# Performance work log

Hardware: AMD Instinct MI355X
Metric: run time of the kernel (lower is better)

The kernel has to match this reference:

```python
import jax, jax.numpy as jnp
import numpy as np

N, C_IN, C_OUT, T, V = 64, 64, 64, 300, 25
INTER_C = C_OUT // 4
NUM_SUBSET = 3
BN_EPS = 1e-5


def setup_inputs() -> dict:
    key = jax.random.key(0)
    ks = jax.random.split(key, 12)
    w_scale = 0.05  # keep attention logits in a sane range
    return {
        "x": jax.random.normal(ks[0], (N, C_IN, T, V), jnp.float32),
        "A": jax.random.uniform(ks[1], (NUM_SUBSET, V, V), jnp.float32),
        "graph_attn": jnp.ones((NUM_SUBSET, V, V), jnp.float32),
        "g_w": jax.random.normal(ks[2], (NUM_SUBSET, C_OUT, C_IN), jnp.float32) * w_scale,
        "g_b": jax.random.normal(ks[3], (NUM_SUBSET, C_OUT), jnp.float32) * w_scale,
        "a_w": jax.random.normal(ks[4], (NUM_SUBSET, INTER_C, C_IN), jnp.float32) * w_scale,
        "a_b": jax.random.normal(ks[5], (NUM_SUBSET, INTER_C), jnp.float32) * w_scale,
        "b_w": jax.random.normal(ks[6], (NUM_SUBSET, INTER_C, C_IN), jnp.float32) * w_scale,
        "b_b": jax.random.normal(ks[7], (NUM_SUBSET, INTER_C), jnp.float32) * w_scale,
        "bn_gamma": jax.random.uniform(ks[8], (C_OUT,), jnp.float32, 0.5, 1.5),
        "bn_beta": jax.random.normal(ks[9], (C_OUT,), jnp.float32) * 0.1,
        "bn_mean": jax.random.normal(ks[10], (C_OUT,), jnp.float32) * 0.1,
        "bn_var": jax.random.uniform(ks[11], (C_OUT,), jnp.float32, 0.5, 1.5),
    }


def _conv1x1(x, w, b):
    # 1x1 Conv2d over channel dim of [N, C, T, V]
    return jnp.einsum('nctv,oc->notv', x, w) + b[None, :, None, None]


def reference(x, A, graph_attn, g_w, g_b, a_w, a_b, b_w, b_b,
              bn_gamma, bn_beta, bn_mean, bn_var):
    A_full = A + graph_attn  # [3, V, V]
    hidden = None
    for i in range(NUM_SUBSET):
        A1 = _conv1x1(x, a_w[i], a_b[i]).transpose(0, 3, 1, 2)  # [N, V, inter_c, T]
        A2 = _conv1x1(x, b_w[i], b_b[i])                        # [N, inter_c, T, V]
        # [N, V, W, T] attention logits, softmax over axis -2 (W)
        S = jnp.einsum('nvct,nctw->nvwt', A1, A2) / INTER_C
        S = jax.nn.softmax(S, axis=-2)
        S = S + A_full[i][None, :, :, None]
        # faithful to torch: sum S over its first spatial axis, elementwise on x
        z = _conv1x1(jnp.einsum('nctv,nwvt->nctv', x, S), g_w[i], g_b[i])
        hidden = z if hidden is None else hidden + z
    # inference-mode BatchNorm2d
    inv = jax.lax.rsqrt(bn_var + BN_EPS)
    h = (hidden - bn_mean[None, :, None, None]) * (bn_gamma * inv)[None, :, None, None] \
        + bn_beta[None, :, None, None]
    # in_channels == out_channels -> identity residual
    h = h + x
    return jax.nn.relu(h)
```

## Files before the change

kernel.cpp:

```cpp
#include <hip/hip_runtime.h>
#include <hip/hip_bf16.h>
#include <math.h>


typedef __attribute__((ext_vector_type(8)))  short bf8;
typedef __attribute__((ext_vector_type(4)))  short bf4;
typedef __attribute__((ext_vector_type(4)))  float f4;
typedef __attribute__((ext_vector_type(16))) float f16v;

#define TT    5
#define COLS  125
#define COLSP 128
#define XROW  72
#define PQROW 40

#define WS_AW    0
#define WS_BW    6144
#define WS_GW    12288
#define WS_COLA  36864
#define WS_SCL   37376
#define WS_SHF   37632
#define WS_END   37888

__device__ __forceinline__ short f2bf(float f) {
  __hip_bfloat16 h = __float2bfloat16(f);
  return __builtin_bit_cast(short, h);
}
__device__ __forceinline__ float bf2f(short s) {
  union { unsigned u; float f; } v;
  v.u = ((unsigned)(unsigned short)s) << 16;
  return v.f;
}
__device__ __forceinline__ float rsum16(float v) {
  v += __shfl_xor(v, 1);
  v += __shfl_xor(v, 2);
  v += __shfl_xor(v, 4);
  v += __shfl_xor(v, 8);
  return v;
}

__global__ void tagc_prep(
    const float* __restrict__ A,    const float* __restrict__ G,
    const float* __restrict__ g_w,  const float* __restrict__ g_b,
    const float* __restrict__ a_w,  const float* __restrict__ b_w,
    const float* __restrict__ bn_g, const float* __restrict__ bn_b,
    const float* __restrict__ bn_m, const float* __restrict__ bn_v,
    short* __restrict__ aw_bf, short* __restrict__ bw_bf,
    short* __restrict__ gw_bf, float* __restrict__ colA3,
    float* __restrict__ scl,   float* __restrict__ shf2)
{
  const int b = blockIdx.x, tid = threadIdx.x;
  if (b < 12) {
    int base = b * 1024 + tid * 4;
    f4 v = *(const f4*)(g_w + base);
    bf4 o;
    #pragma unroll
    for (int r = 0; r < 4; ++r) o[r] = f2bf(v[r]);
    *(bf4*)(gw_bf + base) = o;
  } else if (b == 12) {
    #pragma unroll
    for (int g = 0; g < 3; ++g) {
      int base = g * 1024 + tid * 4;
      f4 v = *(const f4*)(a_w + base);
      bf4 o;
      #pragma unroll
      for (int r = 0; r < 4; ++r) o[r] = f2bf(v[r]);
      *(bf4*)(aw_bf + base) = o;
    }
  } else if (b == 13) {
    #pragma unroll
    for (int g = 0; g < 3; ++g) {
      int base = g * 1024 + tid * 4;
      f4 v = *(const f4*)(b_w + base);
      bf4 o;
      #pragma unroll
      for (int r = 0; r < 4; ++r) o[r] = f2bf(v[r]);
      *(bf4*)(bw_bf + base) = o;
    }
  } else if (b == 14) {
    if (tid < 75) {
      int i = tid / 25, v = tid - 25 * i;
      float s = 0.f;
      for (int a = 0; a < 25; ++a)
        s += A[i * 625 + a * 25 + v] + G[i * 625 + a * 25 + v];
      colA3[tid] = s;
    }
  } else {
    if (tid < 64) {
      float sc  = bn_g[tid] * rsqrtf(bn_v[tid] + 1e-5f);
      float gbs = g_b[tid] + g_b[64 + tid] + g_b[128 + tid];
      scl[tid]  = sc;
      shf2[tid] = bn_b[tid] - bn_m[tid] * sc + gbs * sc;
    }
  }
}

__launch_bounds__(256, 5)
__global__ void tagc_v5_kernel(
    const float* __restrict__ x,
    const float* __restrict__ a_b,
    const float* __restrict__ b_b,
    const short* __restrict__ aw_bf,
    const short* __restrict__ bw_bf,
    const short* __restrict__ gw_bf,
    const float* __restrict__ colA3,
    const float* __restrict__ sclp,
    const float* __restrict__ shf2p,
    float* __restrict__ out)
{
  __shared__ __align__(16) short Xb[COLSP * XROW];
  __shared__ __align__(16) short PQt[COLSP * PQROW];
  __shared__ float sv[TT * 28];
  __shared__ float colA[75];

  const int tid  = threadIdx.x;
  const int wave = tid >> 6;
  const int lane = tid & 63;
  const int l15  = lane & 15;
  const int quad = lane >> 4;
  const int l31  = lane & 31;
  const int hl   = lane >> 5;

  const int lin = blockIdx.y * 60 + blockIdx.x;
  const int idx = lin >> 3;
  const int n   = ((lin & 7) << 3) + idx / 60;
  const int t0  = (idx % 60) * TT;

  if (tid < 75) colA[tid] = colA3[tid];

  {
    const float* xb = x + (long)n * 480000 + t0 * 25;
    #pragma unroll
    for (int k = 0; k < 8; ++k) {
      int idxs = k * 256 + tid;
      int c4  = idxs >> 7;
      int col = idxs & 127;
      bool ok = (col < COLS);
      bf4 wv;
      #pragma unroll
      for (int j = 0; j < 4; ++j) {
        float g = ok ? xb[(4 * c4 + j) * 7500 + col] : 0.f;
        wv[j] = f2bf(g);
      }
      *(bf4*)&Xb[col * XROW + 4 * c4] = wv;
    }
  }

  f16v R0, R1;
  #pragma unroll
  for (int r = 0; r < 16; ++r) { R0[r] = 0.f; R1[r] = 0.f; }

  __syncthreads();

  for (int i = 0; i < 3; ++i) {
    {
      const int mt  = wave & 1;
      const int ntb = (wave >> 1) * 4;
      const short* Wb = (mt ? bw_bf : aw_bf) + i * 1024;
      const float* Bv = (mt ? b_b : a_b) + i * 16;

      bf8 Af[2];
      Af[0] = *(const bf8*)(Wb + l15 * 64 + quad * 8);
      Af[1] = *(const bf8*)(Wb + l15 * 64 + 32 + quad * 8);

      float bias[4];
      #pragma unroll
      for (int r = 0; r < 4; ++r) bias[r] = Bv[quad * 4 + r];

      #pragma unroll
      for (int j = 0; j < 4; ++j) {
        int nt = ntb + j;
        bf8 B0 = *(const bf8*)&Xb[(nt * 16 + l15) * XROW + quad * 8];
        bf8 B1 = *(const bf8*)&Xb[(nt * 16 + l15) * XROW + 32 + quad * 8];
        f4 acc = {0.f, 0.f, 0.f, 0.f};
        acc = __builtin_amdgcn_mfma_f32_16x16x32_bf16(Af[0], B0, acc, 0, 0, 0);
        acc = __builtin_amdgcn_mfma_f32_16x16x32_bf16(Af[1], B1, acc, 0, 0, 0);
        int col = nt * 16 + l15;
        bf4 w;
        #pragma unroll
        for (int r = 0; r < 4; ++r) w[r] = f2bf(acc[r] + bias[r]);
        *(bf4*)&PQt[col * PQROW + mt * 16 + quad * 4] = w;
      }
    }
    __syncthreads();

    for (int tsel = wave; tsel < TT; tsel += 4) {
      f4 sacc[2][2];
      #pragma unroll
      for (int am = 0; am < 2; ++am) {
        bf8 Afr = {0,0,0,0,0,0,0,0};
        if (quad < 2 && (am * 16 + l15) < 25)
          Afr = *(const bf8*)&PQt[(tsel * 25 + am * 16 + l15) * PQROW + quad * 8];
        #pragma unroll
        for (int wm = 0; wm < 2; ++wm) {
          bf8 Bfr = {0,0,0,0,0,0,0,0};
          if (quad < 2 && (wm * 16 + l15) < 25)
            Bfr = *(const bf8*)&PQt[(tsel * 25 + wm * 16 + l15) * PQROW + 16 + quad * 8];
          f4 z = {0.f, 0.f, 0.f, 0.f};
          sacc[am][wm] = __builtin_amdgcn_mfma_f32_16x16x32_bf16(Afr, Bfr, z, 0, 0, 0);
        }
      }
      const bool w1ok = (l15 < 9);
      float cs0 = 0.f, cs1 = 0.f;
      #pragma unroll
      for (int am = 0; am < 2; ++am) {
        #pragma unroll
        for (int r = 0; r < 4; ++r) {
          float e0 = __expf(sacc[am][0][r] * 0.0625f);
          float e1 = w1ok ? __expf(sacc[am][1][r] * 0.0625f) : 0.f;
          float d  = rsum16(e0 + e1);
          float rd = 1.f / d;
          int a = am * 16 + quad * 4 + r;
          if (a < 25) { cs0 += e0 * rd; cs1 += e1 * rd; }
        }
      }
      cs0 += __shfl_xor(cs0, 16); cs0 += __shfl_xor(cs0, 32);
      cs1 += __shfl_xor(cs1, 16); cs1 += __shfl_xor(cs1, 32);
      if (quad == 0) {
        sv[tsel * 28 + l15] = cs0 + colA[i * 25 + l15];
        if (l15 < 9)
          sv[tsel * 28 + 16 + l15] = cs1 + colA[i * 25 + 16 + l15];
      }
    }
    __syncthreads();

    {
      const int trow = wave >> 1;
      const int tcb  = wave & 1;
      const short* gp = gw_bf + i * 4096 + (trow * 32 + l31) * 64;
      bf8 Ag[4];
      #pragma unroll
      for (int kk = 0; kk < 4; ++kk)
        Ag[kk] = *(const bf8*)(gp + kk * 16 + hl * 8);

      #pragma unroll
      for (int tix = 0; tix < 2; ++tix) {
        int colb = (tcb + tix * 2) * 32;
        f16v za;
        #pragma unroll
        for (int r = 0; r < 16; ++r) za[r] = 0.f;
        #pragma unroll
        for (int kk = 0; kk < 4; ++kk) {
          bf8 Bf = *(const bf8*)&Xb[(colb + l31) * XROW + kk * 16 + hl * 8];
          za = __builtin_amdgcn_mfma_f32_32x32x16_bf16(Ag[kk], Bf, za, 0, 0, 0);
        }
        int col  = colb + l31;
        int colc = col < COLS ? col : (COLS - 1);
        int t = colc / 25, v = colc - 25 * t;
        float sval = sv[t * 28 + v];
        if (tix == 0) {
          #pragma unroll
          for (int r = 0; r < 16; ++r) R0[r] += za[r] * sval;
        } else {
          #pragma unroll
          for (int r = 0; r < 16; ++r) R1[r] += za[r] * sval;
        }
      }
    }
  }

  {
    const int trow = wave >> 1;
    const int tcb  = wave & 1;
    float* obase = out + (long)n * 480000 + t0 * 25;
    #pragma unroll
    for (int rg = 0; rg < 4; ++rg) {
      int ob = trow * 32 + rg * 8 + hl * 4;
      f4 sc = *(const f4*)(sclp + ob);
      f4 sh = *(const f4*)(shf2p + ob);
      #pragma unroll
      for (int tix = 0; tix < 2; ++tix) {
        int col = (tcb + tix * 2) * 32 + l31;
        if (col < COLS) {
          bf4 res = *(const bf4*)&Xb[col * XROW + ob];
          #pragma unroll
          for (int r = 0; r < 4; ++r) {
            float acc = tix ? R1[rg * 4 + r] : R0[rg * 4 + r];
            float h = acc * sc[r] + sh[r] + bf2f(res[r]);
            obase[(long)(ob + r) * 7500 + col] = fmaxf(h, 0.f);
          }
        }
      }
    }
  }
}

extern "C" void kernel_launch(void* const* d_in, const int* in_sizes, int n_in,
                              void* d_out, int out_size, void* d_ws, size_t ws_size,
                              hipStream_t stream) {
  (void)in_sizes; (void)n_in; (void)ws_size; (void)out_size;
  char* ws = (char*)d_ws;
  short* aw_bf = (short*)(ws + WS_AW);
  short* bw_bf = (short*)(ws + WS_BW);
  short* gw_bf = (short*)(ws + WS_GW);
  float* colA3 = (float*)(ws + WS_COLA);
  float* scl   = (float*)(ws + WS_SCL);
  float* shf2  = (float*)(ws + WS_SHF);

  tagc_prep<<<dim3(16), dim3(256), 0, stream>>>(
      (const float*)d_in[1],  (const float*)d_in[2],
      (const float*)d_in[3],  (const float*)d_in[4],
      (const float*)d_in[5],  (const float*)d_in[7],
      (const float*)d_in[9],  (const float*)d_in[10],
      (const float*)d_in[11], (const float*)d_in[12],
      aw_bf, bw_bf, gw_bf, colA3, scl, shf2);

  dim3 grid(300 / TT, 64);
  tagc_v5_kernel<<<grid, dim3(256), 0, stream>>>(
      (const float*)d_in[0],
      (const float*)d_in[6],  (const float*)d_in[8],
      aw_bf, bw_bf, gw_bf, colA3, scl, shf2,
      (float*)d_out);
}
```

Measured before the change: 329.5 us.

## Give each wave one time step to remove per-subset block barriers

The kernel now covers four time steps per block instead of five, and each wave owns one whole time step (25 joints). That wave computes the attention projections, the softmax column sums and the g-conv for its time step in its own shared-memory slice, so the two __syncthreads per subset and the shared sv array go away. The gw weight fragments are reloaded inside the loop, the shared-memory footprint shrinks, and launch bounds rise to 6 blocks per SIMD. In exchange, 7 of every 32 MFMA columns are padding, the grid holds more blocks, and global stores are narrower.

Result: slower. 588.8 us (+78.7%).

```diff
diff --git a/kernel.cpp b/kernel.cpp
--- a/kernel.cpp
+++ b/kernel.cpp
@@ -8,9 +8,8 @@
 typedef __attribute__((ext_vector_type(4)))  float f4;
 typedef __attribute__((ext_vector_type(16))) float f16v;
 
-#define TT    5
-#define COLS  125
-#define COLSP 128
+#define TT    4
+#define COLS  100
 #define XROW  72
 #define PQROW 40
 
@@ -95,8 +94,8 @@
   }
 }
 
-__launch_bounds__(256, 5)
-__global__ void tagc_v5_kernel(
+__launch_bounds__(256, 6)
+__global__ void tagc_v7_kernel(
     const float* __restrict__ x,
     const float* __restrict__ a_b,
     const float* __restrict__ b_b,
@@ -108,9 +107,8 @@
     const float* __restrict__ shf2p,
     float* __restrict__ out)
 {
-  __shared__ __align__(16) short Xb[COLSP * XROW];
-  __shared__ __align__(16) short PQt[COLSP * PQROW];
-  __shared__ float sv[TT * 28];
+  __shared__ __align__(16) short Xb[COLS * XROW];
+  __shared__ __align__(16) short PQs[TT * 32 * PQROW];
   __shared__ float colA[75];
 
   const int tid  = threadIdx.x;
@@ -121,28 +119,27 @@
   const int l31  = lane & 31;
   const int hl   = lane >> 5;
 
-  const int lin = blockIdx.y * 60 + blockIdx.x;
+  const int lin = blockIdx.y * 75 + blockIdx.x;
   const int idx = lin >> 3;
-  const int n   = ((lin & 7) << 3) + idx / 60;
-  const int t0  = (idx % 60) * TT;
+  const int n   = ((lin & 7) << 3) + idx / 75;
+  const int t0  = (idx % 75) * TT;
 
   if (tid < 75) colA[tid] = colA3[tid];
 
   {
     const float* xb = x + (long)n * 480000 + t0 * 25;
     #pragma unroll
-    for (int k = 0; k < 8; ++k) {
+    for (int k = 0; k < 7; ++k) {
       int idxs = k * 256 + tid;
-      int c4  = idxs >> 7;
-      int col = idxs & 127;
-      bool ok = (col < COLS);
-      bf4 wv;
-      #pragma unroll
-      for (int j = 0; j < 4; ++j) {
-        float g = ok ? xb[(4 * c4 + j) * 7500 + col] : 0.f;
-        wv[j] = f2bf(g);
-      }
-      *(bf4*)&Xb[col * XROW + 4 * c4] = wv;
+      if (idxs < 1600) {
+        int c4  = idxs / 100;
+        int col = idxs - 100 * c4;
+        bf4 wv;
+        #pragma unroll
+        for (int j = 0; j < 4; ++j)
+          wv[j] = f2bf(xb[(4 * c4 + j) * 7500 + col]);
+        *(bf4*)&Xb[col * XROW + 4 * c4] = wv;
+      }
     }
   }
 
@@ -152,133 +149,113 @@
 
   __syncthreads();
 
+  const int w25 = wave * 25;
+  short* PQw = PQs + wave * (32 * PQROW);
+  const bf8 Z8 = {0,0,0,0,0,0,0,0};
+
   for (int i = 0; i < 3; ++i) {
-    {
-      const int mt  = wave & 1;
-      const int ntb = (wave >> 1) * 4;
+    #pragma unroll
+    for (int mt = 0; mt < 2; ++mt) {
       const short* Wb = (mt ? bw_bf : aw_bf) + i * 1024;
       const float* Bv = (mt ? b_b : a_b) + i * 16;
-
-      bf8 Af[2];
-      Af[0] = *(const bf8*)(Wb + l15 * 64 + quad * 8);
-      Af[1] = *(const bf8*)(Wb + l15 * 64 + 32 + quad * 8);
-
-      float bias[4];
-      #pragma unroll
-      for (int r = 0; r < 4; ++r) bias[r] = Bv[quad * 4 + r];
-
-      #pragma unroll
-      for (int j = 0; j < 4; ++j) {
-        int nt = ntb + j;
-        bf8 B0 = *(const bf8*)&Xb[(nt * 16 + l15) * XROW + quad * 8];
-        bf8 B1 = *(const bf8*)&Xb[(nt * 16 + l15) * XROW + 32 + quad * 8];
+      bf8 W0 = *(const bf8*)(Wb + l15 * 64 + quad * 8);
+      bf8 W1 = *(const bf8*)(Wb + l15 * 64 + 32 + quad * 8);
+      float b0 = Bv[quad * 4 + 0], b1 = Bv[quad * 4 + 1];
+      float b2 = Bv[quad * 4 + 2], b3 = Bv[quad * 4 + 3];
+      #pragma unroll
+      for (int ct = 0; ct < 2; ++ct) {
+        bf8 B0 = Z8, B1 = Z8;
+        if (ct == 0 || l15 < 9) {
+          int row = w25 + ct * 16 + l15;
+          B0 = *(const bf8*)&Xb[row * XROW + quad * 8];
+          B1 = *(const bf8*)&Xb[row * XROW + 32 + quad * 8];
+        }
         f4 acc = {0.f, 0.f, 0.f, 0.f};
-        acc = __builtin_amdgcn_mfma_f32_16x16x32_bf16(Af[0], B0, acc, 0, 0, 0);
-        acc = __builtin_amdgcn_mfma_f32_16x16x32_bf16(Af[1], B1, acc, 0, 0, 0);
-        int col = nt * 16 + l15;
-        bf4 w;
-        #pragma unroll
-        for (int r = 0; r < 4; ++r) w[r] = f2bf(acc[r] + bias[r]);
-        *(bf4*)&PQt[col * PQROW + mt * 16 + quad * 4] = w;
-      }
-    }
-    __syncthreads();
-
-    for (int tsel = wave; tsel < TT; tsel += 4) {
-      f4 sacc[2][2];
-      #pragma unroll
-      for (int am = 0; am < 2; ++am) {
-        bf8 Afr = {0,0,0,0,0,0,0,0};
-        if (quad < 2 && (am * 16 + l15) < 25)
-          Afr = *(const bf8*)&PQt[(tsel * 25 + am * 16 + l15) * PQROW + quad * 8];
-        #pragma unroll
-        for (int wm = 0; wm < 2; ++wm) {
-          bf8 Bfr = {0,0,0,0,0,0,0,0};
-          if (quad < 2 && (wm * 16 + l15) < 25)
-            Bfr = *(const bf8*)&PQt[(tsel * 25 + wm * 16 + l15) * PQROW + 16 + quad * 8];
-          f4 z = {0.f, 0.f, 0.f, 0.f};
-          sacc[am][wm] = __builtin_amdgcn_mfma_f32_16x16x32_bf16(Afr, Bfr, z, 0, 0, 0);
-        }
-      }
-      const bool w1ok = (l15 < 9);
-      float cs0 = 0.f, cs1 = 0.f;
-      #pragma unroll
-      for (int am = 0; am < 2; ++am) {
+        acc = __builtin_amdgcn_mfma_f32_16x16x32_bf16(W0, B0, acc, 0, 0, 0);
+        acc = __builtin_amdgcn_mfma_f32_16x16x32_bf16(W1, B1, acc, 0, 0, 0);
+        bf4 pw;
+        pw[0] = f2bf(acc[0] + b0); pw[1] = f2bf(acc[1] + b1);
+        pw[2] = f2bf(acc[2] + b2); pw[3] = f2bf(acc[3] + b3);
+        *(bf4*)&PQw[(ct * 16 + l15) * PQROW + mt * 16 + quad * 4] = pw;
+      }
+    }
+
+    f4 sacc[2][2];
+    #pragma unroll
+    for (int am = 0; am < 2; ++am) {
+      bf8 Afr = Z8;
+      if (quad < 2 && (am * 16 + l15) < 25)
+        Afr = *(const bf8*)&PQw[(am * 16 + l15) * PQROW + quad * 8];
+      #pragma unroll
+      for (int wm = 0; wm < 2; ++wm) {
+        bf8 Bfr = Z8;
+        if (quad < 2 && (wm * 16 + l15) < 25)
+          Bfr = *(const bf8*)&PQw[(wm * 16 + l15) * PQROW + 16 + quad * 8];
+        f4 z = {0.f, 0.f, 0.f, 0.f};
+        sacc[am][wm] = __builtin_amdgcn_mfma_f32_16x16x32_bf16(Afr, Bfr, z, 0, 0, 0);
+      }
+    }
+    const bool w1ok = (l15 < 9);
+    float cs0 = 0.f, cs1 = 0.f;
+    #pragma unroll
+    for (int am = 0; am < 2; ++am) {
+      #pragma unroll
+      for (int r = 0; r < 4; ++r) {
+        float e0 = __expf(sacc[am][0][r] * 0.0625f);
+        float e1 = w1ok ? __expf(sacc[am][1][r] * 0.0625f) : 0.f;
+        float d  = rsum16(e0 + e1);
+        float rd = 1.f / d;
+        int a = am * 16 + quad * 4 + r;
+        if (a < 25) { cs0 += e0 * rd; cs1 += e1 * rd; }
+      }
+    }
+    cs0 += __shfl_xor(cs0, 16); cs0 += __shfl_xor(cs0, 32);
+    cs1 += __shfl_xor(cs1, 16); cs1 += __shfl_xor(cs1, 32);
+    float sval = 0.f;
+    if (l31 < 25) {
+      float csel = (l31 < 16) ? cs0 : cs1;
+      sval = csel + colA[i * 25 + l31];
+    }
+
+    #pragma unroll
+    for (int tr = 0; tr < 2; ++tr) {
+      f16v za;
+      #pragma unroll
+      for (int r = 0; r < 16; ++r) za[r] = 0.f;
+      #pragma unroll
+      for (int kk = 0; kk < 4; ++kk) {
+        bf8 Bf = Z8;
+        if (l31 < 25)
+          Bf = *(const bf8*)&Xb[(w25 + l31) * XROW + kk * 16 + hl * 8];
+        bf8 Ag = *(const bf8*)(gw_bf + i * 4096 + (tr * 32 + l31) * 64 + kk * 16 + hl * 8);
+        za = __builtin_amdgcn_mfma_f32_32x32x16_bf16(Ag, Bf, za, 0, 0, 0);
+      }
+      if (tr == 0) {
+        #pragma unroll
+        for (int r = 0; r < 16; ++r) R0[r] += za[r] * sval;
+      } else {
+        #pragma unroll
+        for (int r = 0; r < 16; ++r) R1[r] += za[r] * sval;
+      }
+    }
+  }
+
+  if (l31 < 25) {
+    const int col = w25 + l31;
+    float* obase = out + (long)n * 480000 + t0 * 25 + col;
+    #pragma unroll
+    for (int tr = 0; tr < 2; ++tr) {
+      #pragma unroll
+      for (int rg = 0; rg < 4; ++rg) {
+        int ob = tr * 32 + rg * 8 + hl * 4;
+        f4 sc = *(const f4*)(sclp + ob);
+        f4 sh = *(const f4*)(shf2p + ob);
+        bf4 res = *(const bf4*)&Xb[col * XROW + ob];
         #pragma unroll
         for (int r = 0; r < 4; ++r) {
-          float e0 = __expf(sacc[am][0][r] * 0.0625f);
-          float e1 = w1ok ? __expf(sacc[am][1][r] * 0.0625f) : 0.f;
-          float d  = rsum16(e0 + e1);
-          float rd = 1.f / d;
-          int a = am * 16 + quad * 4 + r;
-          if (a < 25) { cs0 += e0 * rd; cs1 += e1 * rd; }
-        }
-      }
-      cs0 += __shfl_xor(cs0, 16); cs0 += __shfl_xor(cs0, 32);
-      cs1 += __shfl_xor(cs1, 16); cs1 += __shfl_xor(cs1, 32);
-      if (quad == 0) {
-        sv[tsel * 28 + l15] = cs0 + colA[i * 25 + l15];
-        if (l15 < 9)
-          sv[tsel * 28 + 16 + l15] = cs1 + colA[i * 25 + 16 + l15];
-      }
-    }
-    __syncthreads();
-
-    {
-      const int trow = wave >> 1;
-      const int tcb  = wave & 1;
-      const short* gp = gw_bf + i * 4096 + (trow * 32 + l31) * 64;
-      bf8 Ag[4];
-      #pragma unroll
-      for (int kk = 0; kk < 4; ++kk)
-        Ag[kk] = *(const bf8*)(gp + kk * 16 + hl * 8);
-
-      #pragma unroll
-      for (int tix = 0; tix < 2; ++tix) {
-        int colb = (tcb + tix * 2) * 32;
-        f16v za;
-        #pragma unroll
-        for (int r = 0; r < 16; ++r) za[r] = 0.f;
-        #pragma unroll
-        for (int kk = 0; kk < 4; ++kk) {
-          bf8 Bf = *(const bf8*)&Xb[(colb + l31) * XROW + kk * 16 + hl * 8];
-          za = __builtin_amdgcn_mfma_f32_32x32x16_bf16(Ag[kk], Bf, za, 0, 0, 0);
-        }
-        int col  = colb + l31;
-        int colc = col < COLS ? col : (COLS - 1);
-        int t = colc / 25, v = colc - 25 * t;
-        float sval = sv[t * 28 + v];
-        if (tix == 0) {
-          #pragma unroll
-          for (int r = 0; r < 16; ++r) R0[r] += za[r] * sval;
-        } else {
-          #pragma unroll
-          for (int r = 0; r < 16; ++r) R1[r] += za[r] * sval;
-        }
-      }
-    }
-  }
-
-  {
-    const int trow = wave >> 1;
-    const int tcb  = wave & 1;
-    float* obase = out + (long)n * 480000 + t0 * 25;
-    #pragma unroll
-    for (int rg = 0; rg < 4; ++rg) {
-      int ob = trow * 32 + rg * 8 + hl * 4;
-      f4 sc = *(const f4*)(sclp + ob);
-      f4 sh = *(const f4*)(shf2p + ob);
-      #pragma unroll
-      for (int tix = 0; tix < 2; ++tix) {
-        int col = (tcb + tix * 2) * 32 + l31;
-        if (col < COLS) {
-          bf4 res = *(const bf4*)&Xb[col * XROW + ob];
-          #pragma unroll
-          for (int r = 0; r < 4; ++r) {
-            float acc = tix ? R1[rg * 4 + r] : R0[rg * 4 + r];
-            float h = acc * sc[r] + sh[r] + bf2f(res[r]);
-            obase[(long)(ob + r) * 7500 + col] = fmaxf(h, 0.f);
-          }
+          float acc = tr ? R1[rg * 4 + r] : R0[rg * 4 + r];
+          float h = acc * sc[r] + sh[r] + bf2f(res[r]);
+          obase[(long)(ob + r) * 7500] = fmaxf(h, 0.f);
         }
       }
     }
@@ -306,7 +283,7 @@
       aw_bf, bw_bf, gw_bf, colA3, scl, shf2);
 
   dim3 grid(300 / TT, 64);
-  tagc_v5_kernel<<<grid, dim3(256), 0, stream>>>(
+  tagc_v7_kernel<<<grid, dim3(256), 0, stream>>>(
       (const float*)d_in[0],
       (const float*)d_in[6],  (const float*)d_in[8],
       aw_bf, bw_bf, gw_bf, colA3, scl, shf2,
```
